# Optimization experiments

Measured on AMD Instinct MI355X. Metric: run time of the kernel, lower is better.

Reference implementation:

```python
import jax, jax.numpy as jnp
import numpy as np

ALPHAS = jnp.array([0.3, 0.7], dtype=jnp.float32)  # registered buffer branch_alphas
SUBSAMPLE = 4
CHUNK = 50


def _cell_step(x_t, h, s, bw, bb, ow, ob):
    """One SimpleDHSRNNCell step.
    x_t: [B, in], h: [B, H], s: [B, K, H] (K=2 branches)
    bw: [K, H, in+H], bb: [K, H], ow: [H, K*H], ob: [H]
    """
    ci = jnp.concatenate([x_t, h], axis=1)                  # [B, in+H]
    bo = jnp.einsum('bi,koi->bko', ci, bw) + bb[None]       # [B, K, H]
    a = ALPHAS[None, :, None]
    ns = a * s + (1.0 - a) * bo                             # new branch states [B, K, H]
    flat = ns.reshape(ns.shape[0], -1)                      # cat branch outputs -> [B, K*H]
    out = jax.nn.relu(flat @ ow.T + ob)                     # spike output [B, H]
    return out, ns


def setup_inputs() -> dict:
    key = jax.random.key(0)
    ks = jax.random.split(key, 11)
    B = 8192

    def lin(k, shape, fan_in):
        lim = 1.0 / np.sqrt(fan_in)
        return jax.random.uniform(k, shape, minval=-lim, maxval=lim, dtype=jnp.float32)

    inp = {
        'x': jax.random.uniform(ks[0], (B, 784, 1), dtype=jnp.float32),
        # rnn1: input 1, hidden 32, 2 branches; branch Linear(33, 32), output Linear(64, 32)
        'r1_bw': lin(ks[1], (2, 32, 33), 33),
        'r1_bb': lin(ks[2], (2, 32), 33),
        'r1_ow': lin(ks[3], (32, 64), 64),
        'r1_ob': lin(ks[4], (32,), 64),
        # rnn2: input 32, hidden 64; branch Linear(96, 64), output Linear(128, 64)
        'r2_bw': lin(ks[5], (2, 64, 96), 96),
        'r2_bb': lin(ks[6], (2, 64), 96),
        'r2_ow': lin(ks[7], (64, 128), 128),
        'r2_ob': lin(ks[8], (64,), 128),
        # classifier Linear(64, 10)
        'cw': lin(ks[9], (10, 64), 64),
        'cb': lin(ks[10], (10,), 64),
    }
    return inp


def reference(x, r1_bw, r1_bb, r1_ow, r1_ob, r2_bw, r2_bb, r2_ow, r2_ob, cw, cb):
    x = x[:, ::SUBSAMPLE, :]                # [B, 196, 1]
    xs = jnp.transpose(x, (1, 0, 2))        # time-major [T, B, 1]
    T, B = xs.shape[0], xs.shape[1]

    def step(carry, x_t):
        h1, s1, h2, s2 = carry
        h1, s1 = _cell_step(x_t, h1, s1, r1_bw, r1_bb, r1_ow, r1_ob)
        h2, s2 = _cell_step(h1, h2, s2, r2_bw, r2_bb, r2_ow, r2_ob)
        return (h1, s1, h2, s2), None

    carry = (jnp.zeros((B, 32), x.dtype), jnp.zeros((B, 2, 32), x.dtype),
             jnp.zeros((B, 64), x.dtype), jnp.zeros((B, 2, 64), x.dtype))
    # chunked processing with detach between chunks (truncated BPTT)
    for start in range(0, T, CHUNK):
        carry = jax.tree_util.tree_map(jax.lax.stop_gradient, carry)
        carry, _ = jax.lax.scan(step, carry, xs[start:min(start + CHUNK, T)])

    h2 = carry[2]                           # final spike output of rnn2 [B, 64]
    return h2 @ cw.T + cb                   # logits [B, 10]
```

## Files before the change

### kernel.cpp

```cpp
#include <hip/hip_runtime.h>


typedef float    f32x4 __attribute__((ext_vector_type(4)));
typedef _Float16 f16x8 __attribute__((ext_vector_type(8)));

#define MFMA16F(a, b, c) __builtin_amdgcn_mfma_f32_16x16x32_f16((a), (b), (c), 0, 0, 0)
#define T_STEPS 196
#define S1S 40
#define S2S 72
#define H1B (16 * S1S)
#define H2B (16 * S2S)

#define WS_M1H 0
#define WS_M1X 2048
#define WS_C1  2112
#define WS_M2  2176
#define WS_C2  14464
#define WS_TOTAL 14592

__global__ void prep_fuse(const float* __restrict__ r1_bw, const float* __restrict__ r1_bb,
                          const float* __restrict__ r1_ow, const float* __restrict__ r2_bw,
                          const float* __restrict__ r2_bb, const float* __restrict__ r2_ow,
                          float* __restrict__ ws)
{
    int idx = blockIdx.x * 256 + threadIdx.x;
    if (idx >= WS_TOTAL) return;
    float acc = 0.0f;
    float sc;
    if (idx < WS_M1X) {
        int kb = idx >> 10, rem = idx & 1023, n = rem >> 5, k = rem & 31;
        sc = kb ? 0.3f : 0.7f;
        for (int j = 0; j < 32; ++j)
            acc += r1_ow[n * 64 + kb * 32 + j] * r1_bw[(kb * 32 + j) * 33 + 1 + k];
    } else if (idx < WS_C1) {
        int r = idx - WS_M1X; int kb = r >> 5, n = r & 31;
        sc = kb ? 0.3f : 0.7f;
        for (int j = 0; j < 32; ++j)
            acc += r1_ow[n * 64 + kb * 32 + j] * r1_bw[(kb * 32 + j) * 33];
    } else if (idx < WS_M2) {
        int r = idx - WS_C1; int kb = r >> 5, n = r & 31;
        sc = kb ? 0.3f : 0.7f;
        for (int j = 0; j < 32; ++j)
            acc += r1_ow[n * 64 + kb * 32 + j] * r1_bb[kb * 32 + j];
    } else if (idx < WS_C2) {
        int r = idx - WS_M2; int kb = r / 6144; int r2 = r - kb * 6144;
        int n = r2 / 96, k = r2 - n * 96;
        sc = kb ? 0.3f : 0.7f;
        for (int j = 0; j < 64; ++j)
            acc += r2_ow[n * 128 + kb * 64 + j] * r2_bw[(kb * 64 + j) * 96 + k];
    } else {
        int r = idx - WS_C2; int kb = r >> 6, n = r & 63;
        sc = kb ? 0.3f : 0.7f;
        for (int j = 0; j < 64; ++j)
            acc += r2_ow[n * 128 + kb * 64 + j] * r2_bb[kb * 64 + j];
    }
    ws[idx] = acc * sc;
}

__device__ __forceinline__ f16x8 cvt8(const float* __restrict__ p) {
    f16x8 o;
#pragma unroll
    for (int i = 0; i < 8; ++i) o[i] = (_Float16)p[i];
    return o;
}

__global__ __launch_bounds__(256, 2)
void dhsrnn_f16(const float* __restrict__ x, const float* __restrict__ ws,
                const float* __restrict__ r1_ob, const float* __restrict__ r2_ob,
                const float* __restrict__ cw, const float* __restrict__ cb,
                float* __restrict__ out)
{
    __shared__ __align__(16) _Float16 H1[2 * H1B];
    __shared__ __align__(16) _Float16 H2[2 * H2B];
    __shared__ float XBuf[2][16];
    __shared__ float hcf[16 * 68];

    const int tid = threadIdx.x;
    const int w   = tid >> 6;
    const int l   = tid & 63;
    const int li  = l & 15;
    const int g   = l >> 4;
    const int row0 = blockIdx.x * 16;

    const int n4 = w * 16 + li;
    f16x8 B2a[3], B2b[3];
#pragma unroll
    for (int kt = 0; kt < 3; ++kt) {
        B2a[kt] = cvt8(ws + WS_M2 + 0 * 6144 + n4 * 96 + kt * 32 + g * 8);
        B2b[kt] = cvt8(ws + WS_M2 + 1 * 6144 + n4 * 96 + kt * 32 + g * 8);
    }
    const float c2a = ws[WS_C2 + n4], c2b = ws[WS_C2 + 64 + n4];
    const float ob2n = r2_ob[n4];
    const f32x4 ci2a = {c2a, c2a, c2a, c2a};
    const f32x4 ci2b = {c2b, c2b, c2b, c2b};

    const int n2 = (w & 1) * 16 + li;
    f16x8 B1a, B1b;
    float m1xa = 0.f, m1xb = 0.f, c1a = 0.f, c1b = 0.f, ob1n = 0.f;
    if (w >= 2) {
        B1a = cvt8(ws + WS_M1H + 0 * 1024 + n2 * 32 + g * 8);
        B1b = cvt8(ws + WS_M1H + 1 * 1024 + n2 * 32 + g * 8);
        m1xa = ws[WS_M1X + n2];      m1xb = ws[WS_M1X + 32 + n2];
        c1a  = ws[WS_C1 + n2];       c1b  = ws[WS_C1 + 32 + n2];
        ob1n = r1_ob[n2];
    }
    const f32x4 ci1a = {c1a, c1a, c1a, c1a};
    const f32x4 ci1b = {c1b, c1b, c1b, c1b};

    f32x4 va  = {0.f, 0.f, 0.f, 0.f}, vb  = {0.f, 0.f, 0.f, 0.f};
    f32x4 va2 = {0.f, 0.f, 0.f, 0.f}, vb2 = {0.f, 0.f, 0.f, 0.f};

    for (int i = tid; i < H2B; i += 256) H2[i] = (_Float16)0.0f;
    if (tid < 16) {
        XBuf[0][tid] = x[(row0 + tid) * 784];
        XBuf[1][tid] = x[(row0 + tid) * 784 + 4];
    }
    __syncthreads();

    if (w >= 2) {
        const f32x4 xv = *reinterpret_cast<const f32x4*>(&XBuf[0][4 * g]);
#pragma unroll
        for (int r = 0; r < 4; ++r) {
            int m = 4 * g + r;
            va[r] = c1a + m1xa * xv[r];
            vb[r] = c1b + m1xb * xv[r];
            float h = fmaxf(va[r] + vb[r] + ob1n, 0.0f);
            H1[m * S1S + n2] = (_Float16)h;
        }
    }
    __syncthreads();

    auto step = [&](const int rb, const int t) {
        const int wb = rb ^ 1;

        float xnext = 0.0f;
        if (w == 0 && l < 16 && t < T_STEPS - 2)
            xnext = x[(row0 + l) * 784 + 4 * (t + 2)];

        const f16x8 a1   = *reinterpret_cast<const f16x8*>(&H1[rb * H1B + li * S1S + g * 8]);
        const f16x8 a2k1 = *reinterpret_cast<const f16x8*>(&H2[rb * H2B + li * S2S + g * 8]);
        const f16x8 a2k2 = *reinterpret_cast<const f16x8*>(&H2[rb * H2B + li * S2S + 32 + g * 8]);

        __builtin_amdgcn_s_setprio(1);
        f32x4 d = MFMA16F(a1, B2a[0], ci2a);
        f32x4 e = MFMA16F(a1, B2b[0], ci2b);
        d = MFMA16F(a2k1, B2a[1], d);
        e = MFMA16F(a2k1, B2b[1], e);
        d = MFMA16F(a2k2, B2a[2], d);
        e = MFMA16F(a2k2, B2b[2], e);
        __builtin_amdgcn_s_setprio(0);
#pragma unroll
        for (int r = 0; r < 4; ++r) {
            int m = 4 * g + r;
            va2[r] = fmaf(0.3f, va2[r], d[r]);
            vb2[r] = fmaf(0.7f, vb2[r], e[r]);
            float h = fmaxf(va2[r] + vb2[r] + ob2n, 0.0f);
            H2[wb * H2B + m * S2S + n4] = (_Float16)h;
        }

        if (w >= 2) {
            __builtin_amdgcn_s_setprio(1);
            f32x4 p = MFMA16F(a1, B1a, ci1a);
            f32x4 q = MFMA16F(a1, B1b, ci1b);
            __builtin_amdgcn_s_setprio(0);
            const f32x4 xv = *reinterpret_cast<const f32x4*>(&XBuf[wb][4 * g]);
#pragma unroll
            for (int r = 0; r < 4; ++r) {
                int m = 4 * g + r;
                float za = fmaf(m1xa, xv[r], p[r]);
                float zb = fmaf(m1xb, xv[r], q[r]);
                va[r] = fmaf(0.3f, va[r], za);
                vb[r] = fmaf(0.7f, vb[r], zb);
                float h = fmaxf(va[r] + vb[r] + ob1n, 0.0f);
                H1[wb * H1B + m * S1S + n2] = (_Float16)h;
            }
        }

        if (w == 0 && l < 16 && t < T_STEPS - 2) XBuf[rb][l] = xnext;
        __syncthreads();
    };

#pragma unroll 1
    for (int tp = 0; tp < (T_STEPS - 2) / 2; ++tp) {
        step(0, 2 * tp);
        step(1, 2 * tp + 1);
    }
    step(0, T_STEPS - 2);

    {
        const int rb = 1;
        const f16x8 a1   = *reinterpret_cast<const f16x8*>(&H1[rb * H1B + li * S1S + g * 8]);
        const f16x8 a2k1 = *reinterpret_cast<const f16x8*>(&H2[rb * H2B + li * S2S + g * 8]);
        const f16x8 a2k2 = *reinterpret_cast<const f16x8*>(&H2[rb * H2B + li * S2S + 32 + g * 8]);
        f32x4 d = MFMA16F(a1, B2a[0], ci2a);
        f32x4 e = MFMA16F(a1, B2b[0], ci2b);
        d = MFMA16F(a2k1, B2a[1], d);
        e = MFMA16F(a2k1, B2b[1], e);
        d = MFMA16F(a2k2, B2a[2], d);
        e = MFMA16F(a2k2, B2b[2], e);
#pragma unroll
        for (int r = 0; r < 4; ++r) {
            int m = 4 * g + r;
            va2[r] = fmaf(0.3f, va2[r], d[r]);
            vb2[r] = fmaf(0.7f, vb2[r], e[r]);
            hcf[m * 68 + n4] = fmaxf(va2[r] + vb2[r] + ob2n, 0.0f);
        }
    }
    __syncthreads();

    {
        const int c = tid >> 4;
        const int e = tid & 15;
        if (c < 10) {
            float acc = cb[c];
#pragma unroll 4
            for (int dd = 0; dd < 64; ++dd)
                acc += hcf[e * 68 + dd] * cw[c * 64 + dd];
            out[(row0 + e) * 10 + c] = acc;
        }
    }
}

extern "C" void kernel_launch(void* const* d_in, const int* in_sizes, int n_in,
                              void* d_out, int out_size, void* d_ws, size_t ws_size,
                              hipStream_t stream) {
    const float* x     = (const float*)d_in[0];
    const float* r1_bw = (const float*)d_in[1];
    const float* r1_bb = (const float*)d_in[2];
    const float* r1_ow = (const float*)d_in[3];
    const float* r1_ob = (const float*)d_in[4];
    const float* r2_bw = (const float*)d_in[5];
    const float* r2_bb = (const float*)d_in[6];
    const float* r2_ow = (const float*)d_in[7];
    const float* r2_ob = (const float*)d_in[8];
    const float* cw    = (const float*)d_in[9];
    const float* cb    = (const float*)d_in[10];
    float* ws  = (float*)d_ws;
    float* out = (float*)d_out;

    hipLaunchKernelGGL(prep_fuse, dim3((WS_TOTAL + 255) / 256), dim3(256), 0, stream,
                       r1_bw, r1_bb, r1_ow, r2_bw, r2_bb, r2_ow, ws);
    hipLaunchKernelGGL(dhsrnn_f16, dim3(512), dim3(256), 0, stream,
                       x, ws, r1_ob, r2_ob, cw, cb, out);
}
```

Measured before the change: 89.27 us.

## Process two 16-row tiles per block to interleave independent recurrences

Each block now handles 32 batch rows as two independent 16-row tiles, with interleaved MFMA chains so the two recurrences hide each other's latency. The grid shrinks to 256 blocks, one per CU, and launch bounds drop to one block per SIMD group. Output biases are folded into the MFMA accumulator init and the state init, removing one add per element per step. The cost is fewer blocks, so any CU without work sits idle, plus more registers and LDS per block.

```diff
diff --git a/kernel.cpp b/kernel.cpp
--- a/kernel.cpp
+++ b/kernel.cpp
@@ -64,23 +64,23 @@
     return o;
 }
 
-__global__ __launch_bounds__(256, 2)
+__global__ __launch_bounds__(256, 1)
 void dhsrnn_f16(const float* __restrict__ x, const float* __restrict__ ws,
                 const float* __restrict__ r1_ob, const float* __restrict__ r2_ob,
                 const float* __restrict__ cw, const float* __restrict__ cb,
                 float* __restrict__ out)
 {
-    __shared__ __align__(16) _Float16 H1[2 * H1B];
-    __shared__ __align__(16) _Float16 H2[2 * H2B];
-    __shared__ float XBuf[2][16];
-    __shared__ float hcf[16 * 68];
+    __shared__ __align__(16) _Float16 H1[4 * H1B];
+    __shared__ __align__(16) _Float16 H2[4 * H2B];
+    __shared__ float XBuf[2][32];
+    __shared__ float hcf[32 * 68];
 
     const int tid = threadIdx.x;
     const int w   = tid >> 6;
     const int l   = tid & 63;
     const int li  = l & 15;
     const int g   = l >> 4;
-    const int row0 = blockIdx.x * 16;
+    const int row0 = blockIdx.x * 32;
 
     const int n4 = w * 16 + li;
     f16x8 B2a[3], B2b[3];
@@ -89,10 +89,11 @@
         B2a[kt] = cvt8(ws + WS_M2 + 0 * 6144 + n4 * 96 + kt * 32 + g * 8);
         B2b[kt] = cvt8(ws + WS_M2 + 1 * 6144 + n4 * 96 + kt * 32 + g * 8);
     }
-    const float c2a = ws[WS_C2 + n4], c2b = ws[WS_C2 + 64 + n4];
     const float ob2n = r2_ob[n4];
-    const f32x4 ci2a = {c2a, c2a, c2a, c2a};
-    const f32x4 ci2b = {c2b, c2b, c2b, c2b};
+    const float c2av = ws[WS_C2 + n4] + 0.7f * ob2n;
+    const float c2bv = ws[WS_C2 + 64 + n4];
+    const f32x4 ci2a = {c2av, c2av, c2av, c2av};
+    const f32x4 ci2b = {c2bv, c2bv, c2bv, c2bv};
 
     const int n2 = (w & 1) * 16 + li;
     f16x8 B1a, B1b;
@@ -104,28 +105,34 @@
         c1a  = ws[WS_C1 + n2];       c1b  = ws[WS_C1 + 32 + n2];
         ob1n = r1_ob[n2];
     }
-    const f32x4 ci1a = {c1a, c1a, c1a, c1a};
+    const float c1av = c1a + 0.7f * ob1n;
+    const f32x4 ci1a = {c1av, c1av, c1av, c1av};
     const f32x4 ci1b = {c1b, c1b, c1b, c1b};
 
-    f32x4 va  = {0.f, 0.f, 0.f, 0.f}, vb  = {0.f, 0.f, 0.f, 0.f};
-    f32x4 va2 = {0.f, 0.f, 0.f, 0.f}, vb2 = {0.f, 0.f, 0.f, 0.f};
-
-    for (int i = tid; i < H2B; i += 256) H2[i] = (_Float16)0.0f;
-    if (tid < 16) {
+    f32x4 vaA = {0.f,0.f,0.f,0.f}, vbA = {0.f,0.f,0.f,0.f};
+    f32x4 vaB = {0.f,0.f,0.f,0.f}, vbB = {0.f,0.f,0.f,0.f};
+    f32x4 va2A = {ob2n, ob2n, ob2n, ob2n}, vb2A = {0.f,0.f,0.f,0.f};
+    f32x4 va2B = {ob2n, ob2n, ob2n, ob2n}, vb2B = {0.f,0.f,0.f,0.f};
+
+    for (int i = tid; i < 2 * H2B; i += 256) H2[i] = (_Float16)0.0f;
+    if (tid < 32) {
         XBuf[0][tid] = x[(row0 + tid) * 784];
         XBuf[1][tid] = x[(row0 + tid) * 784 + 4];
     }
     __syncthreads();
 
     if (w >= 2) {
-        const f32x4 xv = *reinterpret_cast<const f32x4*>(&XBuf[0][4 * g]);
+        const f32x4 xvA = *reinterpret_cast<const f32x4*>(&XBuf[0][4 * g]);
+        const f32x4 xvB = *reinterpret_cast<const f32x4*>(&XBuf[0][16 + 4 * g]);
 #pragma unroll
         for (int r = 0; r < 4; ++r) {
             int m = 4 * g + r;
-            va[r] = c1a + m1xa * xv[r];
-            vb[r] = c1b + m1xb * xv[r];
-            float h = fmaxf(va[r] + vb[r] + ob1n, 0.0f);
-            H1[m * S1S + n2] = (_Float16)h;
+            vaA[r] = c1a + m1xa * xvA[r] + ob1n;
+            vbA[r] = c1b + m1xb * xvA[r];
+            H1[0 * H1B + m * S1S + n2] = (_Float16)fmaxf(vaA[r] + vbA[r], 0.0f);
+            vaB[r] = c1a + m1xa * xvB[r] + ob1n;
+            vbB[r] = c1b + m1xb * xvB[r];
+            H1[1 * H1B + m * S1S + n2] = (_Float16)fmaxf(vaB[r] + vbB[r], 0.0f);
         }
     }
     __syncthreads();
@@ -134,49 +141,67 @@
         const int wb = rb ^ 1;
 
         float xnext = 0.0f;
-        if (w == 0 && l < 16 && t < T_STEPS - 2)
+        if (w == 0 && l < 32 && t < T_STEPS - 2)
             xnext = x[(row0 + l) * 784 + 4 * (t + 2)];
 
-        const f16x8 a1   = *reinterpret_cast<const f16x8*>(&H1[rb * H1B + li * S1S + g * 8]);
-        const f16x8 a2k1 = *reinterpret_cast<const f16x8*>(&H2[rb * H2B + li * S2S + g * 8]);
-        const f16x8 a2k2 = *reinterpret_cast<const f16x8*>(&H2[rb * H2B + li * S2S + 32 + g * 8]);
+        const f16x8 a1A   = *reinterpret_cast<const f16x8*>(&H1[(rb*2+0)*H1B + li*S1S + g*8]);
+        const f16x8 a1B   = *reinterpret_cast<const f16x8*>(&H1[(rb*2+1)*H1B + li*S1S + g*8]);
+        const f16x8 a2k1A = *reinterpret_cast<const f16x8*>(&H2[(rb*2+0)*H2B + li*S2S + g*8]);
+        const f16x8 a2k2A = *reinterpret_cast<const f16x8*>(&H2[(rb*2+0)*H2B + li*S2S + 32 + g*8]);
+        const f16x8 a2k1B = *reinterpret_cast<const f16x8*>(&H2[(rb*2+1)*H2B + li*S2S + g*8]);
+        const f16x8 a2k2B = *reinterpret_cast<const f16x8*>(&H2[(rb*2+1)*H2B + li*S2S + 32 + g*8]);
 
         __builtin_amdgcn_s_setprio(1);
-        f32x4 d = MFMA16F(a1, B2a[0], ci2a);
-        f32x4 e = MFMA16F(a1, B2b[0], ci2b);
-        d = MFMA16F(a2k1, B2a[1], d);
-        e = MFMA16F(a2k1, B2b[1], e);
-        d = MFMA16F(a2k2, B2a[2], d);
-        e = MFMA16F(a2k2, B2b[2], e);
+        f32x4 dA = MFMA16F(a1A, B2a[0], ci2a);
+        f32x4 eA = MFMA16F(a1A, B2b[0], ci2b);
+        f32x4 dB = MFMA16F(a1B, B2a[0], ci2a);
+        f32x4 eB = MFMA16F(a1B, B2b[0], ci2b);
+        dA = MFMA16F(a2k1A, B2a[1], dA);
+        eA = MFMA16F(a2k1A, B2b[1], eA);
+        dB = MFMA16F(a2k1B, B2a[1], dB);
+        eB = MFMA16F(a2k1B, B2b[1], eB);
+        dA = MFMA16F(a2k2A, B2a[2], dA);
+        eA = MFMA16F(a2k2A, B2b[2], eA);
+        dB = MFMA16F(a2k2B, B2a[2], dB);
+        eB = MFMA16F(a2k2B, B2b[2], eB);
         __builtin_amdgcn_s_setprio(0);
 #pragma unroll
         for (int r = 0; r < 4; ++r) {
             int m = 4 * g + r;
-            va2[r] = fmaf(0.3f, va2[r], d[r]);
-            vb2[r] = fmaf(0.7f, vb2[r], e[r]);
-            float h = fmaxf(va2[r] + vb2[r] + ob2n, 0.0f);
-            H2[wb * H2B + m * S2S + n4] = (_Float16)h;
+            va2A[r] = fmaf(0.3f, va2A[r], dA[r]);
+            vb2A[r] = fmaf(0.7f, vb2A[r], eA[r]);
+            H2[(wb*2+0)*H2B + m*S2S + n4] = (_Float16)fmaxf(va2A[r] + vb2A[r], 0.0f);
+            va2B[r] = fmaf(0.3f, va2B[r], dB[r]);
+            vb2B[r] = fmaf(0.7f, vb2B[r], eB[r]);
+            H2[(wb*2+1)*H2B + m*S2S + n4] = (_Float16)fmaxf(va2B[r] + vb2B[r], 0.0f);
         }
 
         if (w >= 2) {
             __builtin_amdgcn_s_setprio(1);
-            f32x4 p = MFMA16F(a1, B1a, ci1a);
-            f32x4 q = MFMA16F(a1, B1b, ci1b);
+            f32x4 pA = MFMA16F(a1A, B1a, ci1a);
+            f32x4 qA = MFMA16F(a1A, B1b, ci1b);
+            f32x4 pB = MFMA16F(a1B, B1a, ci1a);
+            f32x4 qB = MFMA16F(a1B, B1b, ci1b);
             __builtin_amdgcn_s_setprio(0);
-            const f32x4 xv = *reinterpret_cast<const f32x4*>(&XBuf[wb][4 * g]);
+            const f32x4 xvA = *reinterpret_cast<const f32x4*>(&XBuf[wb][4 * g]);
+            const f32x4 xvB = *reinterpret_cast<const f32x4*>(&XBuf[wb][16 + 4 * g]);
 #pragma unroll
             for (int r = 0; r < 4; ++r) {
                 int m = 4 * g + r;
-                float za = fmaf(m1xa, xv[r], p[r]);
-                float zb = fmaf(m1xb, xv[r], q[r]);
-                va[r] = fmaf(0.3f, va[r], za);
-                vb[r] = fmaf(0.7f, vb[r], zb);
-                float h = fmaxf(va[r] + vb[r] + ob1n, 0.0f);
-                H1[wb * H1B + m * S1S + n2] = (_Float16)h;
+                float zaA = fmaf(m1xa, xvA[r], pA[r]);
+                float zbA = fmaf(m1xb, xvA[r], qA[r]);
+                vaA[r] = fmaf(0.3f, vaA[r], zaA);
+                vbA[r] = fmaf(0.7f, vbA[r], zbA);
+                H1[(wb*2+0)*H1B + m*S1S + n2] = (_Float16)fmaxf(vaA[r] + vbA[r], 0.0f);
+                float zaB = fmaf(m1xa, xvB[r], pB[r]);
+                float zbB = fmaf(m1xb, xvB[r], qB[r]);
+                vaB[r] = fmaf(0.3f, vaB[r], zaB);
+                vbB[r] = fmaf(0.7f, vbB[r], zbB);
+                H1[(wb*2+1)*H1B + m*S1S + n2] = (_Float16)fmaxf(vaB[r] + vbB[r], 0.0f);
             }
         }
 
-        if (w == 0 && l < 16 && t < T_STEPS - 2) XBuf[rb][l] = xnext;
+        if (w == 0 && l < 32 && t < T_STEPS - 2) XBuf[rb][l] = xnext;
         __syncthreads();
     };
 
@@ -189,29 +214,41 @@
 
     {
         const int rb = 1;
-        const f16x8 a1   = *reinterpret_cast<const f16x8*>(&H1[rb * H1B + li * S1S + g * 8]);
-        const f16x8 a2k1 = *reinterpret_cast<const f16x8*>(&H2[rb * H2B + li * S2S + g * 8]);
-        const f16x8 a2k2 = *reinterpret_cast<const f16x8*>(&H2[rb * H2B + li * S2S + 32 + g * 8]);
-        f32x4 d = MFMA16F(a1, B2a[0], ci2a);
-        f32x4 e = MFMA16F(a1, B2b[0], ci2b);
-        d = MFMA16F(a2k1, B2a[1], d);
-        e = MFMA16F(a2k1, B2b[1], e);
-        d = MFMA16F(a2k2, B2a[2], d);
-        e = MFMA16F(a2k2, B2b[2], e);
+        const f16x8 a1A   = *reinterpret_cast<const f16x8*>(&H1[(rb*2+0)*H1B + li*S1S + g*8]);
+        const f16x8 a1B   = *reinterpret_cast<const f16x8*>(&H1[(rb*2+1)*H1B + li*S1S + g*8]);
+        const f16x8 a2k1A = *reinterpret_cast<const f16x8*>(&H2[(rb*2+0)*H2B + li*S2S + g*8]);
+        const f16x8 a2k2A = *reinterpret_cast<const f16x8*>(&H2[(rb*2+0)*H2B + li*S2S + 32 + g*8]);
+        const f16x8 a2k1B = *reinterpret_cast<const f16x8*>(&H2[(rb*2+1)*H2B + li*S2S + g*8]);
+        const f16x8 a2k2B = *reinterpret_cast<const f16x8*>(&H2[(rb*2+1)*H2B + li*S2S + 32 + g*8]);
+        f32x4 dA = MFMA16F(a1A, B2a[0], ci2a);
+        f32x4 eA = MFMA16F(a1A, B2b[0], ci2b);
+        f32x4 dB = MFMA16F(a1B, B2a[0], ci2a);
+        f32x4 eB = MFMA16F(a1B, B2b[0], ci2b);
+        dA = MFMA16F(a2k1A, B2a[1], dA);
+        eA = MFMA16F(a2k1A, B2b[1], eA);
+        dB = MFMA16F(a2k1B, B2a[1], dB);
+        eB = MFMA16F(a2k1B, B2b[1], eB);
+        dA = MFMA16F(a2k2A, B2a[2], dA);
+        eA = MFMA16F(a2k2A, B2b[2], eA);
+        dB = MFMA16F(a2k2B, B2a[2], dB);
+        eB = MFMA16F(a2k2B, B2b[2], eB);
 #pragma unroll
         for (int r = 0; r < 4; ++r) {
             int m = 4 * g + r;
-            va2[r] = fmaf(0.3f, va2[r], d[r]);
-            vb2[r] = fmaf(0.7f, vb2[r], e[r]);
-            hcf[m * 68 + n4] = fmaxf(va2[r] + vb2[r] + ob2n, 0.0f);
+            va2A[r] = fmaf(0.3f, va2A[r], dA[r]);
+            vb2A[r] = fmaf(0.7f, vb2A[r], eA[r]);
+            hcf[(0 * 16 + m) * 68 + n4] = fmaxf(va2A[r] + vb2A[r], 0.0f);
+            va2B[r] = fmaf(0.3f, va2B[r], dB[r]);
+            vb2B[r] = fmaf(0.7f, vb2B[r], eB[r]);
+            hcf[(1 * 16 + m) * 68 + n4] = fmaxf(va2B[r] + vb2B[r], 0.0f);
         }
     }
     __syncthreads();
 
     {
-        const int c = tid >> 4;
-        const int e = tid & 15;
-        if (c < 10) {
+        const int e = tid & 31;
+#pragma unroll 1
+        for (int c = tid >> 5; c < 10; c += 8) {
             float acc = cb[c];
 #pragma unroll 4
             for (int dd = 0; dd < 64; ++dd)
@@ -240,6 +277,6 @@
 
     hipLaunchKernelGGL(prep_fuse, dim3((WS_TOTAL + 255) / 256), dim3(256), 0, stream,
                        r1_bw, r1_bb, r1_ow, r2_bw, r2_bb, r2_ow, ws);
-    hipLaunchKernelGGL(dhsrnn_f16, dim3(512), dim3(256), 0, stream,
+    hipLaunchKernelGGL(dhsrnn_f16, dim3(256), dim3(256), 0, stream,
                        x, ws, r1_ob, r2_ob, cw, cb, out);
 }
```

Measured after the change: 124.7 us. 1.4x slower.
